# Kernel optimization log

Hardware: AMD Instinct MI355X
Metric: run time of the kernel (lower is better)

Reference implementation:

```python
import jax, jax.numpy as jnp
import numpy as np

NEG_BIG = -9.0e15


def masked_mean_softmax(idx):
    # softmax over a 0/-inf mask == uniform weights over positions where idx > 0
    logits = jnp.where(idx > 0, 1.0, NEG_BIG).astype(jnp.float32)
    return jax.nn.softmax(logits, axis=1)


def setup_inputs() -> dict:
    key = jax.random.key(0)
    ks = jax.random.split(key, 8)
    N_NODES, N_EDGES, EDGE_ARITY, NODE_DEG = 100000, 50000, 32, 16
    D_IN, D_OUT, TV = 128, 128, 128
    stdv = 1.0 / np.sqrt(D_IN)
    u = lambda k, shp: jax.random.uniform(k, shp, jnp.float32, -stdv, stdv)
    return {
        "x": jax.random.normal(ks[0], (N_NODES, D_IN), jnp.float32),
        "seq": jax.random.randint(ks[1], (N_EDGES, EDGE_ARITY), 0, N_NODES),
        "useq": jax.random.randint(ks[2], (N_NODES, NODE_DEG), 0, N_EDGES),
        "TextVector": jax.random.normal(ks[3], (TV,), jnp.float32),
        "weight1": u(ks[4], (D_IN, D_OUT)),
        "weight2": u(ks[5], (D_OUT, D_OUT)),
        "weight3": u(ks[6], (TV, TV)),
    }


def reference(x, seq, useq, TextVector, weight1, weight2, weight3):
    # NOTE: the torch module overwrites TextVector with weight3[0]; dropout is
    # a no-op in eval mode and is omitted here.
    tv = weight3[0]                                   # [TV]
    dot = weight3 @ tv                                # [TV]
    cos = dot / (jnp.linalg.norm(tv) * jnp.linalg.norm(weight3, axis=1))
    inter_nw = jnp.mean(cos)                          # scalar

    xw = (x @ weight1) * inter_nw                     # [N, D_OUT]

    nor = masked_mean_softmax(seq)                    # [E, A]
    adj_with_fea = xw[seq]                            # [E, A, D_OUT] gather
    edge = jnp.einsum('eac,ea->ec', adj_with_fea, nor)
    edge = jax.nn.relu(edge)
    e1 = edge @ weight2                               # [E, D_OUT]

    u_nor = masked_mean_softmax(useq)                 # [N, K]
    edge_adj = e1[useq]                               # [N, K, D_OUT] gather
    node = jnp.einsum('nkc,nk->nc', edge_adj, u_nor)  # [N, D_OUT]
    return node
```

## Files before the change

### kernel.cpp

```cpp
#include <hip/hip_runtime.h>
#include <hip/hip_fp16.h>

#define ND 100000
#define NE 50000
#define AR 32
#define DG 16
#define D  128

typedef _Float16 half8_t __attribute__((ext_vector_type(8)));
typedef _Float16 half4_t __attribute__((ext_vector_type(4)));
typedef float    f32x4_t __attribute__((ext_vector_type(4)));

#define APAD 136

__global__ __launch_bounds__(256) void k_prep(const float* __restrict__ w1,
                                              const float* __restrict__ w2,
                                              const float* __restrict__ w3,
                                              _Float16* __restrict__ w1f,
                                              _Float16* __restrict__ w2f,
                                              float* __restrict__ inter_out) {
    if (blockIdx.x == 64) {
        __shared__ float red[128];
        int j = threadIdx.x;
        if (j < 128) {
            float dot = 0.f, sq = 0.f, sq0 = 0.f;
            #pragma unroll 8
            for (int k = 0; k < D; ++k) {
                float wj = w3[j * D + k];
                float w0 = w3[k];
                dot += wj * w0;
                sq  += wj * wj;
                sq0 += w0 * w0;
            }
            red[j] = dot / (sqrtf(sq0) * sqrtf(sq));
        }
        __syncthreads();
        if (j == 0) {
            float s = 0.f;
            for (int i = 0; i < 128; ++i) s += red[i];
            inter_out[0] = s / 128.f;
        }
        return;
    }
    int o = blockIdx.x * 256 + threadIdx.x;
    int j    = o & 7;
    int lane = (o >> 3) & 63;
    int frag = o >> 9;
    int ntile = frag >> 2, ktile = frag & 3;
    int n = ntile * 16 + (lane & 15);
    int k = ktile * 32 + (lane >> 4) * 8 + j;
    w1f[o] = (_Float16)w1[k * D + n];
    w2f[o] = (_Float16)w2[k * D + n];
}

__global__ __launch_bounds__(256) void k_xw(const float* __restrict__ x,
                                            const _Float16* __restrict__ w1f_g,
                                            const float* __restrict__ inter_p,
                                            _Float16* __restrict__ xwh) {
    __shared__ _Float16 wfrag[D * D];
    __shared__ _Float16 xs[64 * APAD];
    int t = threadIdx.x;

    {
        const float4* src = (const float4*)w1f_g;
        float4* dst = (float4*)wfrag;
        #pragma unroll
        for (int i = 0; i < 8; ++i) dst[i * 256 + t] = src[i * 256 + t];
    }
    int rowbase = blockIdx.x * 64;
    #pragma unroll
    for (int p = 0; p < 8; ++p) {
        int idx = p * 1024 + t * 4;
        int r = idx >> 7, c = idx & 127;
        int grow = rowbase + r;
        float4 v = make_float4(0.f, 0.f, 0.f, 0.f);
        if (grow < ND) v = ((const float4*)x)[(size_t)grow * 32 + (c >> 2)];
        half4_t h = { (_Float16)v.x, (_Float16)v.y, (_Float16)v.z, (_Float16)v.w };
        *(half4_t*)&xs[r * APAD + c] = h;
    }
    __syncthreads();

    int wave = t >> 6, lane = t & 63;
    int quad = lane >> 4, l15 = lane & 15;
    int m0 = wave * 16;
    float inter = inter_p[0];

    half8_t a[4];
    #pragma unroll
    for (int kt = 0; kt < 4; ++kt)
        a[kt] = *(const half8_t*)&xs[(m0 + l15) * APAD + kt * 32 + quad * 8];

    #pragma unroll
    for (int nt = 0; nt < 8; ++nt) {
        f32x4_t acc = {0.f, 0.f, 0.f, 0.f};
        #pragma unroll
        for (int kt = 0; kt < 4; ++kt) {
            half8_t b = *(const half8_t*)&wfrag[((nt * 4 + kt) * 64 + lane) * 8];
            acc = __builtin_amdgcn_mfma_f32_16x16x32_f16(a[kt], b, acc, 0, 0, 0);
        }
        int col = nt * 16 + l15;
        #pragma unroll
        for (int i = 0; i < 4; ++i) {
            int grow = rowbase + m0 + quad * 4 + i;
            if (grow < ND)
                xwh[(size_t)grow * D + col] = (_Float16)(acc[i] * inter);
        }
    }
}

__global__ __launch_bounds__(256) void k_gather_e(const int* __restrict__ seq,
                                                  const _Float16* __restrict__ xwh,
                                                  _Float16* __restrict__ ea) {
    int t = threadIdx.x;
    int wave = t >> 6, lane = t & 63;
    int e = blockIdx.x * 4 + wave;
    int grp = lane >> 4, il = lane & 15;

    int sval = seq[(size_t)e * AR + (lane & 31)];
    unsigned long long b = __ballot(sval > 0);
    int cnt = __popcll((unsigned long long)(b & 0xffffffffULL));
    const float wuni = 1.f / 32.f;
    float wv = (cnt > 0) ? 1.f / (float)cnt : wuni;

    float acc[8] = {};
    #pragma unroll
    for (int i = 0; i < 8; ++i) {
        int aslot = i * 4 + grp;
        int srow = __shfl(sval, aslot, 64);
        float wa = (cnt > 0) ? ((srow > 0) ? wv : 0.f) : wuni;
        half8_t v = *(const half8_t*)(xwh + (size_t)srow * D + il * 8);
        #pragma unroll
        for (int jj = 0; jj < 8; ++jj) acc[jj] = fmaf(wa, (float)v[jj], acc[jj]);
    }
    #pragma unroll
    for (int jj = 0; jj < 8; ++jj) {
        acc[jj] += __shfl_down(acc[jj], 32, 64);
        acc[jj] += __shfl_down(acc[jj], 16, 64);
    }
    if (lane < 16) {
        half8_t h;
        #pragma unroll
        for (int jj = 0; jj < 8; ++jj) h[jj] = (_Float16)fmaxf(acc[jj], 0.f);
        *(half8_t*)(ea + (size_t)e * D + il * 8) = h;
    }
}

__global__ __launch_bounds__(256) void k_gemm_e(const _Float16* __restrict__ ea,
                                                const _Float16* __restrict__ w2f_g,
                                                _Float16* __restrict__ e1h) {
    __shared__ _Float16 wfrag[D * D];
    __shared__ _Float16 et[64 * APAD];
    int t = threadIdx.x;
    {
        const float4* src = (const float4*)w2f_g;
        float4* dst = (float4*)wfrag;
        #pragma unroll
        for (int i = 0; i < 8; ++i) dst[i * 256 + t] = src[i * 256 + t];
    }
    int rowbase = blockIdx.x * 64;
    #pragma unroll
    for (int p = 0; p < 4; ++p) {
        int hidx = p * 2048 + t * 8;
        int r = hidx >> 7, c = hidx & 127;
        int grow = rowbase + r;
        int gs = (grow < NE) ? grow : (NE - 1);
        half8_t v = *(const half8_t*)(ea + (size_t)gs * D + c);
        *(half8_t*)&et[r * APAD + c] = v;
    }
    __syncthreads();

    int wave = t >> 6, lane = t & 63;
    int quad = lane >> 4, l15 = lane & 15;
    int m0 = wave * 16;

    half8_t a[4];
    #pragma unroll
    for (int kt = 0; kt < 4; ++kt)
        a[kt] = *(const half8_t*)&et[(m0 + l15) * APAD + kt * 32 + quad * 8];

    #pragma unroll
    for (int nt = 0; nt < 8; ++nt) {
        f32x4_t acc = {0.f, 0.f, 0.f, 0.f};
        #pragma unroll
        for (int kt = 0; kt < 4; ++kt) {
            half8_t b = *(const half8_t*)&wfrag[((nt * 4 + kt) * 64 + lane) * 8];
            acc = __builtin_amdgcn_mfma_f32_16x16x32_f16(a[kt], b, acc, 0, 0, 0);
        }
        int col = nt * 16 + l15;
        #pragma unroll
        for (int i = 0; i < 4; ++i) {
            int grow = rowbase + m0 + quad * 4 + i;
            if (grow < NE)
                e1h[(size_t)grow * D + col] = (_Float16)acc[i];
        }
    }
}

__global__ __launch_bounds__(256) void k_gather_n(const int* __restrict__ useq,
                                                  const _Float16* __restrict__ e1h,
                                                  float* __restrict__ out) {
    int t = threadIdx.x;
    int wave = t >> 6, lane = t & 63;
    int n0 = blockIdx.x * 8 + wave * 2;
    int n1 = n0 + 1;
    int grp = lane >> 4, il = lane & 15;

    int nd = grp & 1;
    int sval = useq[(size_t)(n0 + nd) * DG + il];
    unsigned long long b = __ballot(sval > 0);
    int cnt0 = __popcll((unsigned long long)(b & 0xFFFFULL));
    int cnt1 = __popcll((unsigned long long)((b >> 16) & 0xFFFFULL));
    const float wuni = 1.f / 16.f;
    float wv0 = (cnt0 > 0) ? 1.f / (float)cnt0 : wuni;
    float wv1 = (cnt1 > 0) ? 1.f / (float)cnt1 : wuni;

    float acc0[8] = {}, acc1[8] = {};
    #pragma unroll
    for (int i = 0; i < 4; ++i) {
        int slot = i * 4 + grp;
        int s0 = __shfl(sval, slot, 64);
        int s1 = __shfl(sval, 16 + slot, 64);
        float w0 = (cnt0 > 0) ? ((s0 > 0) ? wv0 : 0.f) : wuni;
        float w1 = (cnt1 > 0) ? ((s1 > 0) ? wv1 : 0.f) : wuni;
        half8_t v0 = *(const half8_t*)(e1h + (size_t)s0 * D + il * 8);
        half8_t v1 = *(const half8_t*)(e1h + (size_t)s1 * D + il * 8);
        #pragma unroll
        for (int jj = 0; jj < 8; ++jj) {
            acc0[jj] = fmaf(w0, (float)v0[jj], acc0[jj]);
            acc1[jj] = fmaf(w1, (float)v1[jj], acc1[jj]);
        }
    }
    #pragma unroll
    for (int jj = 0; jj < 8; ++jj) {
        acc0[jj] += __shfl_down(acc0[jj], 32, 64);
        acc0[jj] += __shfl_down(acc0[jj], 16, 64);
        acc1[jj] += __shfl_down(acc1[jj], 32, 64);
        acc1[jj] += __shfl_down(acc1[jj], 16, 64);
    }
    if (lane < 16) {
        float4 o0a = make_float4(acc0[0], acc0[1], acc0[2], acc0[3]);
        float4 o0b = make_float4(acc0[4], acc0[5], acc0[6], acc0[7]);
        float4 o1a = make_float4(acc1[0], acc1[1], acc1[2], acc1[3]);
        float4 o1b = make_float4(acc1[4], acc1[5], acc1[6], acc1[7]);
        float4* p0 = (float4*)(out + (size_t)n0 * D + il * 8);
        float4* p1 = (float4*)(out + (size_t)n1 * D + il * 8);
        p0[0] = o0a; p0[1] = o0b;
        p1[0] = o1a; p1[1] = o1b;
    }
}

extern "C" void kernel_launch(void* const* d_in, const int* in_sizes, int n_in,
                              void* d_out, int out_size, void* d_ws, size_t ws_size,
                              hipStream_t stream) {
    const float* x    = (const float*)d_in[0];
    const int*   seq  = (const int*)d_in[1];
    const int*   useq = (const int*)d_in[2];
    const float* w1   = (const float*)d_in[4];
    const float* w2   = (const float*)d_in[5];
    const float* w3   = (const float*)d_in[6];
    float* out = (float*)d_out;

    _Float16* xwh   = (_Float16*)d_out;
    _Float16* ea    = (_Float16*)d_out + (size_t)ND * D;
    float*    inter = (float*)d_ws;
    _Float16* w1f   = (_Float16*)((char*)d_ws + 256);
    _Float16* w2f   = (_Float16*)((char*)d_ws + 256 + 32768);
    _Float16* e1h   = (_Float16*)((char*)d_ws + 256 + 65536);

    hipLaunchKernelGGL(k_prep,     dim3(65),             dim3(256), 0, stream, w1, w2, w3, w1f, w2f, inter);
    hipLaunchKernelGGL(k_xw,       dim3((ND + 63) / 64), dim3(256), 0, stream, x, w1f, inter, xwh);
    hipLaunchKernelGGL(k_gather_e, dim3(NE / 4),         dim3(256), 0, stream, seq, xwh, ea);
    hipLaunchKernelGGL(k_gemm_e,   dim3((NE + 63) / 64), dim3(256), 0, stream, ea, w2f, e1h);
    hipLaunchKernelGGL(k_gather_n, dim3(ND / 8),         dim3(256), 0, stream, useq, e1h, out);
}
```

Before: 232.7 us.

## Sort gather indices by memory region per row to improve locality in gather kernels

Both gather kernels are restructured so that a 16-lane group owns one edge or node. The kernel bucket-sorts that row's valid indices into 16 coarse address ranges using ballots, stores them in shared memory, and walks them in sorted order, so concurrent loads hit nearby rows. Invalid slots are pushed to the end and zero-weighted, which removes the cross-lane shuffle reduction. Outputs are written with nontemporal stores. The 17-step ballot loop adds ALU and shared-memory overhead per row, and locality gains across waves are uncertain.

```diff
diff --git a/kernel.cpp b/kernel.cpp
--- a/kernel.cpp
+++ b/kernel.cpp
@@ -60,7 +60,6 @@
     __shared__ _Float16 wfrag[D * D];
     __shared__ _Float16 xs[64 * APAD];
     int t = threadIdx.x;
-
     {
         const float4* src = (const float4*)w1f_g;
         float4* dst = (float4*)wfrag;
@@ -111,38 +110,64 @@
 __global__ __launch_bounds__(256) void k_gather_e(const int* __restrict__ seq,
                                                   const _Float16* __restrict__ xwh,
                                                   _Float16* __restrict__ ea) {
+    __shared__ int srt[16 * AR];
     int t = threadIdx.x;
     int wave = t >> 6, lane = t & 63;
-    int e = blockIdx.x * 4 + wave;
-    int grp = lane >> 4, il = lane & 15;
-
-    int sval = seq[(size_t)e * AR + (lane & 31)];
-    unsigned long long b = __ballot(sval > 0);
-    int cnt = __popcll((unsigned long long)(b & 0xffffffffULL));
-    const float wuni = 1.f / 32.f;
-    float wv = (cnt > 0) ? 1.f / (float)cnt : wuni;
-
-    float acc[8] = {};
-    #pragma unroll
-    for (int i = 0; i < 8; ++i) {
-        int aslot = i * 4 + grp;
-        int srow = __shfl(sval, aslot, 64);
-        float wa = (cnt > 0) ? ((srow > 0) ? wv : 0.f) : wuni;
-        half8_t v = *(const half8_t*)(xwh + (size_t)srow * D + il * 8);
-        #pragma unroll
-        for (int jj = 0; jj < 8; ++jj) acc[jj] = fmaf(wa, (float)v[jj], acc[jj]);
-    }
-    #pragma unroll
-    for (int jj = 0; jj < 8; ++jj) {
-        acc[jj] += __shfl_down(acc[jj], 32, 64);
-        acc[jj] += __shfl_down(acc[jj], 16, 64);
-    }
-    if (lane < 16) {
-        half8_t h;
-        #pragma unroll
-        for (int jj = 0; jj < 8; ++jj) h[jj] = (_Float16)fmaxf(acc[jj], 0.f);
-        *(half8_t*)(ea + (size_t)e * D + il * 8) = h;
-    }
+    int e = lane >> 4, l16 = lane & 15;
+    int le = wave * 4 + e;
+    int eg = blockIdx.x * 16 + le;
+
+    int2 sv = ((const int2*)seq)[(size_t)eg * 16 + l16];
+    int sh = e * 16;
+    unsigned long long b0 = __ballot(sv.x > 0);
+    unsigned long long b1 = __ballot(sv.y > 0);
+    unsigned int f0 = (unsigned int)(b0 >> sh) & 0xFFFFu;
+    unsigned int f1 = (unsigned int)(b1 >> sh) & 0xFFFFu;
+    int cnt = __popc(f0) + __popc(f1);
+    bool allv = (cnt == 0);
+    if (allv) cnt = AR;
+    float wvf = 1.f / (float)cnt;
+    bool v0 = (sv.x > 0) | allv, v1 = (sv.y > 0) | allv;
+    int key0 = v0 ? (sv.x / 6250) : 16;
+    int key1 = v1 ? (sv.y / 6250) : 16;
+
+    unsigned int lowj  = (1u << l16) - 1u;
+    unsigned int lowj1 = lowj | (1u << l16);
+    int off = 0, r0 = 0, r1 = 0;
+    #pragma unroll
+    for (int cv = 0; cv <= 16; ++cv) {
+        unsigned long long m0 = __ballot(key0 == cv);
+        unsigned long long m1 = __ballot(key1 == cv);
+        unsigned int g0 = (unsigned int)(m0 >> sh) & 0xFFFFu;
+        unsigned int g1 = (unsigned int)(m1 >> sh) & 0xFFFFu;
+        if (key0 == cv) r0 = off + __popc(g0 & lowj)  + __popc(g1 & lowj);
+        if (key1 == cv) r1 = off + __popc(g0 & lowj1) + __popc(g1 & lowj);
+        off += __popc(g0) + __popc(g1);
+    }
+    srt[le * AR + r0] = sv.x;
+    srt[le * AR + r1] = sv.y;
+
+    float acc[8] = {0.f, 0.f, 0.f, 0.f, 0.f, 0.f, 0.f, 0.f};
+    int colOff = l16 * 8;
+    #pragma unroll
+    for (int tg = 0; tg < 8; ++tg) {
+        int4 sr = *(const int4*)&srt[le * AR + tg * 4];
+        int rows[4] = { sr.x, sr.y, sr.z, sr.w };
+        #pragma unroll
+        for (int u = 0; u < 4; ++u) {
+            int tt = tg * 4 + u;
+            float w = (tt < cnt) ? wvf : 0.f;
+            half8_t v = *(const half8_t*)(xwh + (size_t)rows[u] * D + colOff);
+            #pragma unroll
+            for (int jj = 0; jj < 8; ++jj)
+                acc[jj] = fmaf(w, (float)v[jj], acc[jj]);
+        }
+    }
+    half8_t h;
+    #pragma unroll
+    for (int jj = 0; jj < 8; ++jj) h[jj] = (_Float16)fmaxf(acc[jj], 0.f);
+    f32x4_t hv = *(f32x4_t*)&h;
+    __builtin_nontemporal_store(hv, (f32x4_t*)(ea + (size_t)eg * D + colOff));
 }
 
 __global__ __launch_bounds__(256) void k_gemm_e(const _Float16* __restrict__ ea,
@@ -199,54 +224,56 @@
 __global__ __launch_bounds__(256) void k_gather_n(const int* __restrict__ useq,
                                                   const _Float16* __restrict__ e1h,
                                                   float* __restrict__ out) {
+    __shared__ int srt[16 * DG];
     int t = threadIdx.x;
     int wave = t >> 6, lane = t & 63;
-    int n0 = blockIdx.x * 8 + wave * 2;
-    int n1 = n0 + 1;
-    int grp = lane >> 4, il = lane & 15;
-
-    int nd = grp & 1;
-    int sval = useq[(size_t)(n0 + nd) * DG + il];
+    int nd = lane >> 4, l16 = lane & 15;
+    int ln = wave * 4 + nd;
+    int ng = blockIdx.x * 16 + ln;
+
+    int sval = useq[(size_t)ng * DG + l16];
+    int sh = nd * 16;
     unsigned long long b = __ballot(sval > 0);
-    int cnt0 = __popcll((unsigned long long)(b & 0xFFFFULL));
-    int cnt1 = __popcll((unsigned long long)((b >> 16) & 0xFFFFULL));
-    const float wuni = 1.f / 16.f;
-    float wv0 = (cnt0 > 0) ? 1.f / (float)cnt0 : wuni;
-    float wv1 = (cnt1 > 0) ? 1.f / (float)cnt1 : wuni;
-
-    float acc0[8] = {}, acc1[8] = {};
-    #pragma unroll
-    for (int i = 0; i < 4; ++i) {
-        int slot = i * 4 + grp;
-        int s0 = __shfl(sval, slot, 64);
-        int s1 = __shfl(sval, 16 + slot, 64);
-        float w0 = (cnt0 > 0) ? ((s0 > 0) ? wv0 : 0.f) : wuni;
-        float w1 = (cnt1 > 0) ? ((s1 > 0) ? wv1 : 0.f) : wuni;
-        half8_t v0 = *(const half8_t*)(e1h + (size_t)s0 * D + il * 8);
-        half8_t v1 = *(const half8_t*)(e1h + (size_t)s1 * D + il * 8);
-        #pragma unroll
-        for (int jj = 0; jj < 8; ++jj) {
-            acc0[jj] = fmaf(w0, (float)v0[jj], acc0[jj]);
-            acc1[jj] = fmaf(w1, (float)v1[jj], acc1[jj]);
-        }
-    }
-    #pragma unroll
-    for (int jj = 0; jj < 8; ++jj) {
-        acc0[jj] += __shfl_down(acc0[jj], 32, 64);
-        acc0[jj] += __shfl_down(acc0[jj], 16, 64);
-        acc1[jj] += __shfl_down(acc1[jj], 32, 64);
-        acc1[jj] += __shfl_down(acc1[jj], 16, 64);
-    }
-    if (lane < 16) {
-        float4 o0a = make_float4(acc0[0], acc0[1], acc0[2], acc0[3]);
-        float4 o0b = make_float4(acc0[4], acc0[5], acc0[6], acc0[7]);
-        float4 o1a = make_float4(acc1[0], acc1[1], acc1[2], acc1[3]);
-        float4 o1b = make_float4(acc1[4], acc1[5], acc1[6], acc1[7]);
-        float4* p0 = (float4*)(out + (size_t)n0 * D + il * 8);
-        float4* p1 = (float4*)(out + (size_t)n1 * D + il * 8);
-        p0[0] = o0a; p0[1] = o0b;
-        p1[0] = o1a; p1[1] = o1b;
-    }
+    unsigned int f = (unsigned int)(b >> sh) & 0xFFFFu;
+    int cnt = __popc(f);
+    bool allv = (cnt == 0);
+    if (allv) cnt = DG;
+    float wvf = 1.f / (float)cnt;
+    bool v = (sval > 0) | allv;
+    int key = v ? (sval / 3125) : 16;
+
+    unsigned int lowj = (1u << l16) - 1u;
+    int off = 0, r = 0;
+    #pragma unroll
+    for (int cv = 0; cv <= 16; ++cv) {
+        unsigned long long m = __ballot(key == cv);
+        unsigned int g = (unsigned int)(m >> sh) & 0xFFFFu;
+        if (key == cv) r = off + __popc(g & lowj);
+        off += __popc(g);
+    }
+    srt[ln * DG + r] = sval;
+
+    float acc[8] = {0.f, 0.f, 0.f, 0.f, 0.f, 0.f, 0.f, 0.f};
+    int colOff = l16 * 8;
+    #pragma unroll
+    for (int tg = 0; tg < 4; ++tg) {
+        int4 sr = *(const int4*)&srt[ln * DG + tg * 4];
+        int rows[4] = { sr.x, sr.y, sr.z, sr.w };
+        #pragma unroll
+        for (int u = 0; u < 4; ++u) {
+            int tt = tg * 4 + u;
+            float w = (tt < cnt) ? wvf : 0.f;
+            half8_t vv = *(const half8_t*)(e1h + (size_t)rows[u] * D + colOff);
+            #pragma unroll
+            for (int jj = 0; jj < 8; ++jj)
+                acc[jj] = fmaf(w, (float)vv[jj], acc[jj]);
+        }
+    }
+    f32x4_t o0 = { acc[0], acc[1], acc[2], acc[3] };
+    f32x4_t o1 = { acc[4], acc[5], acc[6], acc[7] };
+    f32x4_t* p = (f32x4_t*)(out + (size_t)ng * D + colOff);
+    __builtin_nontemporal_store(o0, p);
+    __builtin_nontemporal_store(o1, p + 1);
 }
 
 extern "C" void kernel_launch(void* const* d_in, const int* in_sizes, int n_in,
@@ -269,7 +296,7 @@
 
     hipLaunchKernelGGL(k_prep,     dim3(65),             dim3(256), 0, stream, w1, w2, w3, w1f, w2f, inter);
     hipLaunchKernelGGL(k_xw,       dim3((ND + 63) / 64), dim3(256), 0, stream, x, w1f, inter, xwh);
-    hipLaunchKernelGGL(k_gather_e, dim3(NE / 4),         dim3(256), 0, stream, seq, xwh, ea);
+    hipLaunchKernelGGL(k_gather_e, dim3(NE / 16),        dim3(256), 0, stream, seq, xwh, ea);
     hipLaunchKernelGGL(k_gemm_e,   dim3((NE + 63) / 64), dim3(256), 0, stream, ea, w2f, e1h);
-    hipLaunchKernelGGL(k_gather_n, dim3(ND / 8),         dim3(256), 0, stream, useq, e1h, out);
-}
+    hipLaunchKernelGGL(k_gather_n, dim3(ND / 16),        dim3(256), 0, stream, useq, e1h, out);
+}
```

Measured after the change: 230.3 us. No clear change (-1.1%).
